# Kernel optimization log

Measured on AMD Instinct MI355X. Metric: run time of the kernel, lower is better.

## Reference

```python
import jax, jax.numpy as jnp
import numpy as np

DIM = 512
HEADS = 16
DIM_HEAD = 64
INNER = HEADS * DIM_HEAD
MAX_T = 32
BASE = 10000.0


def rotate_half(t):
    t1, t2 = jnp.split(t, 2, axis=-1)
    return jnp.concatenate((-t2, t1), axis=-1)


def setup_inputs() -> dict:
    key = jax.random.key(0)
    ks = jax.random.split(key, 12)
    B, T, S = 2, 16, 128
    x = jax.random.normal(ks[0], (B, T, S, DIM), dtype=jnp.float32)
    y = jax.random.normal(ks[1], (B, T, S, DIM), dtype=jnp.float32)
    temporal_mask = jax.random.randint(ks[2], (B, T, T), 0, 2).astype(jnp.int32)
    sc = 1.0 / np.sqrt(DIM)
    Wq = jax.random.normal(ks[3], (DIM, INNER), dtype=jnp.float32) * sc
    Wk = jax.random.normal(ks[4], (DIM, INNER), dtype=jnp.float32) * sc
    Wv = jax.random.normal(ks[5], (DIM, INNER), dtype=jnp.float32) * sc
    Wo = jax.random.normal(ks[6], (INNER, DIM), dtype=jnp.float32) / np.sqrt(INNER)
    bo = jnp.zeros((DIM,), dtype=jnp.float32)
    pos_emb = jax.random.normal(ks[7], (MAX_T, DIM), dtype=jnp.float32)
    gate_w = jax.random.normal(ks[8], (DIM, 1), dtype=jnp.float32) * sc
    gate_b = jnp.zeros((1,), dtype=jnp.float32)
    return {"x": x, "y": y, "temporal_mask": temporal_mask, "Wq": Wq, "Wk": Wk,
            "Wv": Wv, "Wo": Wo, "bo": bo, "pos_emb": pos_emb,
            "gate_w": gate_w, "gate_b": gate_b}


def reference(x, y, temporal_mask, Wq, Wk, Wv, Wo, bo, pos_emb, gate_w, gate_b):
    B, T, S, D = x.shape
    n = T * S
    scale = DIM_HEAD ** (-0.5)
    # temporal positional embedding (T <= MAX_T path)
    tp = pos_emb[:T][None, :, None, :]  # [1,T,1,D]
    x = x + tp
    y = y + tp
    xf = x.reshape(B, n, D)
    yf = y.reshape(B, n, D)
    # NOTE: k is computed from x (as in the source), v from y
    q = (xf @ Wq).reshape(B, n, HEADS, DIM_HEAD).transpose(0, 2, 1, 3)
    k = (xf @ Wk).reshape(B, n, HEADS, DIM_HEAD).transpose(0, 2, 1, 3)
    v = (yf @ Wv).reshape(B, n, HEADS, DIM_HEAD).transpose(0, 2, 1, 3)
    # RoPE over flattened token index
    inv_freq = 1.0 / (BASE ** (jnp.arange(0, DIM_HEAD, 2, dtype=jnp.float32) / DIM_HEAD))
    freqs = jnp.arange(n, dtype=jnp.float32)[:, None] * inv_freq[None, :]  # [n, d/2]
    emb = jnp.concatenate((freqs, freqs), axis=-1)  # [n, d]
    fc = jnp.cos(emb)[None, None, :, :]
    fs = jnp.sin(emb)[None, None, :, :]
    q = q * fc + rotate_half(q) * fs
    k = k * fc + rotate_half(k) * fs
    dots = jnp.einsum('bhid,bhjd->bhij', q, k) * scale  # [B,H,n,n]
    # expand temporal mask [B,T,T] -> [B,1,n,n] block structure
    m = jnp.repeat(jnp.repeat(temporal_mask, S, axis=1), S, axis=2)[:, None, :, :]
    dots = jnp.where(m == 0, -jnp.inf, dots)
    attn = jax.nn.softmax(dots, axis=-1)
    out = jnp.einsum('bhij,bhjd->bhid', attn, v)  # [B,H,n,d]
    out = out.transpose(0, 2, 1, 3).reshape(B, n, INNER)
    out = out @ Wo + bo
    out = out.reshape(B, T, S, D)
    gate = jax.nn.sigmoid(out @ gate_w + gate_b)  # [B,T,S,1]
    return out * gate
```

## Files before the change

### kernel.cpp

```cpp
#include <hip/hip_runtime.h>
#include <hip/hip_bf16.h>

typedef __attribute__((ext_vector_type(4))) short short4v;
typedef __attribute__((ext_vector_type(8))) short short8v;
typedef __attribute__((ext_vector_type(4))) float float4v;
typedef __attribute__((ext_vector_type(2))) unsigned int uint2v;
typedef __attribute__((ext_vector_type(4))) unsigned int uint4v;

#define NTOK 2048
#define MROWS 4096
#define DMODEL 512
#define NINNER 1024
#define DH 64
#define HH 16
#define LOG2E 1.4426950408889634f

__device__ __forceinline__ unsigned short b2s(float f) {
    __hip_bfloat16 h = __float2bfloat16(f);
    return __builtin_bit_cast(unsigned short, h);
}
__device__ __forceinline__ float bf2f(unsigned short h) {
    unsigned int u = ((unsigned int)h) << 16;
    return __builtin_bit_cast(float, u);
}

__device__ __forceinline__ float4v mfma32(short8v a, short8v b, float4v c) {
    return __builtin_amdgcn_mfma_f32_16x16x32_bf16(a, b, c, 0, 0, 0);
}

__device__ __forceinline__ void gld16(const void* g, void* l) {
    __builtin_amdgcn_global_load_lds((const __attribute__((address_space(1))) void*)g,
                                     (__attribute__((address_space(3))) void*)l, 16, 0, 0);
}

__global__ void k_pre(const float* __restrict__ x, const float* __restrict__ y,
                      const float* __restrict__ pe,
                      unsigned short* __restrict__ xpb, unsigned short* __restrict__ ypb,
                      const float* __restrict__ Wq, const float* __restrict__ Wk,
                      const float* __restrict__ Wv, const float* __restrict__ Wo,
                      const float* __restrict__ gwv, const float* __restrict__ gbv,
                      const float* __restrict__ bo,
                      unsigned short* __restrict__ wall, unsigned short* __restrict__ wot,
                      float* __restrict__ ctab, float* __restrict__ stab,
                      unsigned short* __restrict__ gvp, float* __restrict__ bgp) {
    __shared__ float tl[64][65];
    const int blk = blockIdx.x;
    const int tid = threadIdx.x;
    if (blk < 2048) {
        int e0 = (blk * 256 + tid) * 4;
        int row = e0 >> 9, col = e0 & 511;
        int t = (row & (NTOK - 1)) >> 7;
        const float4v xv = *(const float4v*)(x + e0);
        const float4v yv = *(const float4v*)(y + e0);
        const float4v pv = *(const float4v*)(pe + t * DMODEL + col);
        short4v xo, yo;
#pragma unroll
        for (int i = 0; i < 4; ++i) {
            xo[i] = (short)b2s(xv[i] + pv[i]);
            yo[i] = (short)b2s(yv[i] + pv[i]);
        }
        *(short4v*)(xpb + e0) = xo;
        *(short4v*)(ypb + e0) = yo;
    } else if (blk < 2560) {
        int t = blk - 2048;
        const float* W;
        unsigned short* dst;
        int K, N, k0, n0;
        if (t < 384) {
            int which = t / 128, tile = t % 128;
            W = (which == 0) ? Wq : (which == 1) ? Wk : Wv;
            dst = wall + (size_t)which * 1024 * 512;
            K = 512; N = 1024;
            k0 = (tile >> 4) * 64; n0 = (tile & 15) * 64;
        } else {
            int tile = t - 384;
            W = Wo; dst = wot;
            K = 1024; N = 512;
            k0 = (tile >> 3) * 64; n0 = (tile & 7) * 64;
        }
        int tx = tid & 63, ty4 = tid >> 6;
#pragma unroll
        for (int p = 0; p < 16; ++p) {
            int ky = p * 4 + ty4;
            tl[ky][tx] = W[(size_t)(k0 + ky) * N + n0 + tx];
        }
        __syncthreads();
#pragma unroll
        for (int p = 0; p < 16; ++p) {
            int ny = p * 4 + ty4;
            dst[(size_t)(n0 + ny) * K + k0 + tx] = b2s(tl[tx][ny]);
        }
    } else if (blk < 2816) {
        int idx = (blk - 2560) * 256 + tid;
        int p = idx >> 5, j = idx & 31;
        float invf = powf(10000.0f, -(float)(2 * j) * (1.0f / 64.0f));
        float f = (float)p * invf;
        ctab[idx] = cosf(f);
        stab[idx] = sinf(f);
    } else if (blk < 2832) {
        int base = (blk - 2816) * 64;
        int w = tid >> 6, l = tid & 63, l16 = l & 15, g = l >> 4;
        int row = base + w * 16 + l16;
        const float* wr = Wo + (size_t)row * 512 + g * 128;
        const float* gr = gwv + g * 128;
        float s = 0.f;
#pragma unroll
        for (int t = 0; t < 32; ++t) {
            float4v a = *(const float4v*)(wr + t * 4);
            float4v b = *(const float4v*)(gr + t * 4);
            s += a[0] * b[0] + a[1] * b[1] + a[2] * b[2] + a[3] * b[3];
        }
        s += __shfl_xor(s, 16);
        s += __shfl_xor(s, 32);
        if (g == 0) gvp[row] = b2s(s);
    } else {
        if (tid < 64) {
            float s = 0.f;
#pragma unroll
            for (int t = 0; t < 8; ++t) s += bo[tid + t * 64] * gwv[tid + t * 64];
#pragma unroll
            for (int off = 32; off > 0; off >>= 1) s += __shfl_xor(s, off);
            if (tid == 0) bgp[0] = s + gbv[0];
        }
    }
}

__global__ __launch_bounds__(256) void k_qkv(const unsigned short* __restrict__ A,
                                             const unsigned short* __restrict__ A2,
                                             const unsigned short* __restrict__ Bt,
                                             unsigned short* __restrict__ Cq,
                                             unsigned short* __restrict__ Ck,
                                             unsigned short* __restrict__ Cvv,
                                             const float* __restrict__ ctab,
                                             const float* __restrict__ stab,
                                             float scale) {
    __shared__ unsigned short Ab[2][4096];
    __shared__ unsigned short Bb[2][4096];
    const int tid = threadIdx.x;
    const int w = tid >> 6, l = tid & 63, l16 = l & 15, g = l >> 4;
    const int wm = w >> 1, wn = w & 1;
    const int m0 = blockIdx.y * 128, n0 = blockIdx.x * 128;
    const unsigned short* Ap = (n0 >= 2048) ? A2 : A;
    float4v acc[4][4];
#pragma unroll
    for (int i = 0; i < 4; ++i)
#pragma unroll
        for (int j = 0; j < 4; ++j) acc[i][j] = (float4v){0.f, 0.f, 0.f, 0.f};

    auto stage = [&](int t, int buf) {
        int k0 = t * 32;
#pragma unroll
        for (int it = 0; it < 2; ++it) {
            int f = it * 4 + w;
            gld16(Ap + (size_t)(m0 + f * 16 + l16) * 512 + k0 + g * 8, &Ab[buf][f * 512]);
            gld16(Bt + (size_t)(n0 + f * 16 + l16) * 512 + k0 + g * 8, &Bb[buf][f * 512]);
        }
    };

    stage(0, 0);
    __syncthreads();
    for (int t = 0; t < 16; ++t) {
        const int cur = t & 1;
        if (t + 1 < 16) stage(t + 1, cur ^ 1);
        short8v af[4], bf[4];
#pragma unroll
        for (int mi = 0; mi < 4; ++mi)
            af[mi] = *(const short8v*)&Ab[cur][(wm * 4 + mi) * 512 + l * 8];
#pragma unroll
        for (int nj = 0; nj < 4; ++nj)
            bf[nj] = *(const short8v*)&Bb[cur][(wn * 4 + nj) * 512 + l * 8];
        __builtin_amdgcn_s_setprio(1);
#pragma unroll
        for (int mi = 0; mi < 4; ++mi)
#pragma unroll
            for (int nj = 0; nj < 4; ++nj)
                acc[mi][nj] = mfma32(af[mi], bf[nj], acc[mi][nj]);
        __builtin_amdgcn_s_setprio(0);
        __syncthreads();
    }

    const int hh = (n0 + wn * 64) >> 6;
    const int head = hh & 15;
    if (hh < 32) {
        unsigned short* out = (hh < 16) ? Cq : Ck;
        const float sc = (hh < 16) ? scale : 1.0f;
#pragma unroll
        for (int mi = 0; mi < 4; ++mi)
#pragma unroll
            for (int r = 0; r < 4; ++r) {
                int row = m0 + wm * 64 + mi * 16 + g * 4 + r;
                int b = row >> 11, pos = row & (NTOK - 1);
                const float* cr = ctab + pos * 32;
                const float* sr = stab + pos * 32;
                unsigned short* ob = out + (size_t)((b * HH + head) * NTOK + pos) * DH;
#pragma unroll
                for (int nj = 0; nj < 2; ++nj) {
                    int j = nj * 16 + l16;
                    float c = cr[j], s = sr[j];
                    float v1 = acc[mi][nj][r], v2 = acc[mi][nj + 2][r];
                    ob[j] = b2s((v1 * c - v2 * s) * sc);
                    ob[j + 32] = b2s((v2 * c + v1 * s) * sc);
                }
            }
    } else {
#pragma unroll
        for (int mi = 0; mi < 4; ++mi)
#pragma unroll
            for (int nj = 0; nj < 4; ++nj) {
                int d = nj * 16 + l16;
                int row0 = m0 + wm * 64 + mi * 16 + g * 4;
                int b = row0 >> 11, pos0 = row0 & (NTOK - 1);
                short4v o;
#pragma unroll
                for (int r = 0; r < 4; ++r) o[r] = (short)b2s(acc[mi][nj][r]);
                *(short4v*)(Cvv + (size_t)((b * HH + head) * DH + d) * NTOK + pos0) = o;
            }
    }
}

__global__ __launch_bounds__(256) void k_oproj(const unsigned short* __restrict__ A,
                                               const unsigned short* __restrict__ Bt,
                                               const float* __restrict__ bo,
                                               const unsigned short* __restrict__ gv,
                                               const float* __restrict__ bgp,
                                               float* __restrict__ out) {
    __shared__ unsigned short Ab[2][4096];
    __shared__ unsigned short Bb[2][2048];
    __shared__ float glds[128];
    const int tid = threadIdx.x;
    const int w = tid >> 6, l = tid & 63, l16 = l & 15, g = l >> 4;
    const int m0 = blockIdx.y * 128, n0 = blockIdx.x * 64;
    float4v acc[2][4];
#pragma unroll
    for (int i = 0; i < 2; ++i)
#pragma unroll
        for (int j = 0; j < 4; ++j) acc[i][j] = (float4v){0.f, 0.f, 0.f, 0.f};
    float gp0 = 0.f, gp1 = 0.f;

    auto stage = [&](int t, int buf) {
        int k0 = t * 32;
#pragma unroll
        for (int s = 0; s < 2; ++s) {
            int fi = s * 4 + w;
            gld16(A + (size_t)(m0 + fi * 16 + l16) * 1024 + k0 + g * 8, &Ab[buf][fi * 512]);
        }
        gld16(Bt + (size_t)(n0 + w * 16 + l16) * 1024 + k0 + g * 8, &Bb[buf][w * 512]);
    };

    stage(0, 0);
    __syncthreads();
    for (int t = 0; t < 32; ++t) {
        const int cur = t & 1;
        if (t + 1 < 32) stage(t + 1, cur ^ 1);
        short8v af[2], bf[4];
#pragma unroll
        for (int mi = 0; mi < 2; ++mi)
            af[mi] = *(const short8v*)&Ab[cur][(w * 2 + mi) * 512 + l * 8];
#pragma unroll
        for (int nj = 0; nj < 4; ++nj)
            bf[nj] = *(const short8v*)&Bb[cur][nj * 512 + l * 8];
        short8v gvv = *(const short8v*)(gv + t * 32 + g * 8);
        __builtin_amdgcn_s_setprio(1);
#pragma unroll
        for (int mi = 0; mi < 2; ++mi)
#pragma unroll
            for (int nj = 0; nj < 4; ++nj)
                acc[mi][nj] = mfma32(af[mi], bf[nj], acc[mi][nj]);
        __builtin_amdgcn_s_setprio(0);
#pragma unroll
        for (int j = 0; j < 8; ++j) {
            float gf = bf2f((unsigned short)gvv[j]);
            gp0 = fmaf(bf2f((unsigned short)af[0][j]), gf, gp0);
            gp1 = fmaf(bf2f((unsigned short)af[1][j]), gf, gp1);
        }
        __syncthreads();
    }
    gp0 += __shfl_xor(gp0, 16); gp0 += __shfl_xor(gp0, 32);
    gp1 += __shfl_xor(gp1, 16); gp1 += __shfl_xor(gp1, 32);
    const float bg = bgp[0];
    if (g == 0) {
        glds[w * 32 + l16] = 1.0f / (1.0f + __expf(-(gp0 + bg)));
        glds[w * 32 + 16 + l16] = 1.0f / (1.0f + __expf(-(gp1 + bg)));
    }
    __syncthreads();
#pragma unroll
    for (int mi = 0; mi < 2; ++mi)
#pragma unroll
        for (int nj = 0; nj < 4; ++nj) {
            int col = n0 + nj * 16 + l16;
            float bv = bo[col];
#pragma unroll
            for (int r = 0; r < 4; ++r) {
                int row = m0 + w * 32 + mi * 16 + g * 4 + r;
                float gt = glds[w * 32 + mi * 16 + g * 4 + r];
                out[(size_t)row * 512 + col] = (acc[mi][nj][r] + bv) * gt;
            }
        }
}

__global__ __launch_bounds__(512) void k_attn(const unsigned short* __restrict__ qh,
                                              const unsigned short* __restrict__ kh,
                                              const unsigned short* __restrict__ vt,
                                              const int* __restrict__ tmask,
                                              unsigned short* __restrict__ otmp) {
    __shared__ unsigned short Kb[2][8192];
    __shared__ unsigned short Vb[2][8192];
    __shared__ int tlist[17];
    const int blk = blockIdx.x;
    const int u = (blk & 7) * 64 + (blk >> 3);
    const int ti = u & 15, h = (u >> 4) & 15, b = u >> 8;
    const int tid = threadIdx.x, w = tid >> 6, l = tid & 63, l16 = l & 15, g = l >> 4;
    if (tid == 0) {
        int c = 0;
        for (int j = 0; j < 16; ++j)
            if (tmask[(b * 16 + ti) * 16 + j]) tlist[c++] = j;
        tlist[16] = c;
    }
    __syncthreads();
    const int cnt = tlist[16];
    const unsigned short* qb = qh + (size_t)((b * HH + h) * NTOK) * DH;
    const unsigned short* kb = kh + (size_t)((b * HH + h) * NTOK) * DH;
    const unsigned short* vb = vt + (size_t)((b * HH + h) * DH) * NTOK;
    const int q0 = ti * 128 + w * 16;

    short8v qf[2];
#pragma unroll
    for (int c = 0; c < 2; ++c)
        qf[c] = *(const short8v*)(qb + (size_t)(q0 + l16) * DH + c * 32 + g * 8);

    float4v oacc[4];
#pragma unroll
    for (int i = 0; i < 4; ++i) oacc[i] = (float4v){0.f, 0.f, 0.f, 0.f};
    float mx = -1e30f, lrow = 0.f;
    uint4v vrg[2];

    auto stageK = [&](int tj, int buf) {
#pragma unroll
        for (int s = 0; s < 2; ++s) {
            int fi = w * 2 + s;
            const unsigned short* ga =
                kb + (size_t)(tj * 128 + (fi >> 1) * 16 + l16) * DH + (fi & 1) * 32 + g * 8;
            gld16(ga, &Kb[buf][fi * 512]);
        }
    };
    auto loadV = [&](int tj) {
#pragma unroll
        for (int s = 0; s < 2; ++s) {
            int fi = w * 2 + s;
            const unsigned short* ga =
                vb + (size_t)((fi >> 2) * 16 + l16) * NTOK + tj * 128 + (fi & 3) * 32 + g * 4;
            uint2v lo = *(const uint2v*)ga;
            uint2v hi = *(const uint2v*)(ga + 16);
            vrg[s] = (uint4v){lo[0], lo[1], hi[0], hi[1]};
        }
    };
    auto writeV = [&](int buf) {
#pragma unroll
        for (int s = 0; s < 2; ++s)
            *(uint4v*)&Vb[buf][(w * 2 + s) * 512 + l * 8] = vrg[s];
    };

    if (cnt > 0) {
        stageK(tlist[0], 0);
        loadV(tlist[0]);
        writeV(0);
        __syncthreads();
        for (int i = 0; i < cnt; ++i) {
            const int cur = i & 1;
            const bool pre = (i + 1 < cnt);
            if (pre) { stageK(tlist[i + 1], cur ^ 1); loadV(tlist[i + 1]); }
            float4v sacc[8];
#pragma unroll
            for (int jk = 0; jk < 8; ++jk) sacc[jk] = (float4v){0.f, 0.f, 0.f, 0.f};
            __builtin_amdgcn_s_setprio(1);
#pragma unroll
            for (int jk = 0; jk < 8; ++jk) {
                short8v kf0 = *(const short8v*)&Kb[cur][(jk * 2 + 0) * 512 + l * 8];
                short8v kf1 = *(const short8v*)&Kb[cur][(jk * 2 + 1) * 512 + l * 8];
                sacc[jk] = mfma32(kf0, qf[0], sacc[jk]);
                sacc[jk] = mfma32(kf1, qf[1], sacc[jk]);
            }
            __builtin_amdgcn_s_setprio(0);
            float tm = -1e30f;
#pragma unroll
            for (int jk = 0; jk < 8; ++jk) {
                float4v s4 = sacc[jk];
                tm = fmaxf(tm, fmaxf(fmaxf(s4[0], s4[1]), fmaxf(s4[2], s4[3])));
            }
            tm = fmaxf(tm, __shfl_xor(tm, 16));
            tm = fmaxf(tm, __shfl_xor(tm, 32));
            if (!__all(tm <= mx + 8.0f)) {
                float mnew = fmaxf(mx, tm);
                float alpha = exp2f(mx - mnew);
                lrow *= alpha;
#pragma unroll
                for (int md = 0; md < 4; ++md)
#pragma unroll
                    for (int r = 0; r < 4; ++r) oacc[md][r] *= alpha;
                mx = mnew;
            }
            short8v pf[4];
            float4v tsv = {0.f, 0.f, 0.f, 0.f};
#pragma unroll
            for (int cc = 0; cc < 4; ++cc) {
                float p[8];
#pragma unroll
                for (int r = 0; r < 4; ++r) {
                    p[r] = exp2f(sacc[2 * cc][r] - mx);
                    p[r + 4] = exp2f(sacc[2 * cc + 1][r] - mx);
                }
                short8v pv;
#pragma unroll
                for (int r = 0; r < 4; ++r) {
                    tsv[r] += p[r] + p[r + 4];
                    pv[r] = (short)b2s(p[r]);
                    pv[r + 4] = (short)b2s(p[r + 4]);
                }
                pf[cc] = pv;
            }
            float ts = (tsv[0] + tsv[1]) + (tsv[2] + tsv[3]);
            ts += __shfl_xor(ts, 16);
            ts += __shfl_xor(ts, 32);
            lrow += ts;
            if (pre) writeV(cur ^ 1);
            __builtin_amdgcn_s_setprio(1);
#pragma unroll
            for (int md = 0; md < 4; ++md)
#pragma unroll
                for (int cc = 0; cc < 4; ++cc) {
                    short8v vf = *(const short8v*)&Vb[cur][(md * 4 + cc) * 512 + l * 8];
                    oacc[md] = mfma32(vf, pf[cc], oacc[md]);
                }
            __builtin_amdgcn_s_setprio(0);
            __syncthreads();
        }
    }
    float inv = lrow > 0.f ? 1.0f / lrow : 0.f;
    int q = q0 + l16;
#pragma unroll
    for (int md = 0; md < 4; ++md) {
        short4v o;
#pragma unroll
        for (int r = 0; r < 4; ++r) o[r] = (short)b2s(oacc[md][r] * inv);
        *(short4v*)(otmp + (size_t)(b * NTOK + q) * NINNER + h * DH + md * 16 + g * 4) = o;
    }
}

extern "C" void kernel_launch(void* const* d_in, const int* in_sizes, int n_in,
                              void* d_out, int out_size, void* d_ws, size_t ws_size,
                              hipStream_t stream) {
    (void)in_sizes; (void)n_in; (void)out_size; (void)ws_size;
    const float* x = (const float*)d_in[0];
    const float* y = (const float*)d_in[1];
    const int* tmask = (const int*)d_in[2];
    const float* Wq = (const float*)d_in[3];
    const float* Wk = (const float*)d_in[4];
    const float* Wv = (const float*)d_in[5];
    const float* Wo = (const float*)d_in[6];
    const float* bo = (const float*)d_in[7];
    const float* pe = (const float*)d_in[8];
    const float* gw = (const float*)d_in[9];
    const float* gb = (const float*)d_in[10];

    char* ws = (char*)d_ws;
    const size_t MB = 1u << 20;
    unsigned short* xpb  = (unsigned short*)(ws + 0);
    unsigned short* ypb  = (unsigned short*)(ws + 4 * MB);
    unsigned short* wall = (unsigned short*)(ws + 8 * MB);
    unsigned short* wot  = (unsigned short*)(ws + 11 * MB);
    unsigned short* qh   = (unsigned short*)(ws + 12 * MB);
    unsigned short* kh   = (unsigned short*)(ws + 20 * MB);
    unsigned short* vt   = (unsigned short*)(ws + 28 * MB);
    unsigned short* otm  = (unsigned short*)(ws + 36 * MB);
    float* ct = (float*)(ws + 44 * MB);
    float* st = (float*)(ws + 44 * MB + 256 * 1024);
    unsigned short* gv = (unsigned short*)(ws + 45 * MB);
    float* bg = (float*)(ws + 45 * MB + 4096);
    float* outp = (float*)d_out;

    k_pre<<<2833, 256, 0, stream>>>(x, y, pe, xpb, ypb, Wq, Wk, Wv, Wo, gw, gb, bo,
                                    wall, wot, ct, st, gv, bg);
    k_qkv<<<dim3(24, 32), 256, 0, stream>>>(xpb, ypb, wall, qh, kh, vt, ct, st,
                                            0.125f * LOG2E);
    k_attn<<<512, 512, 0, stream>>>(qh, kh, vt, tmask, otm);
    k_oproj<<<dim3(8, 32), 256, 0, stream>>>(otm, wot, bo, gv, bg, outp);
}
```

Baseline: 135.6 us.

## Halve attention KV tile to 64 keys and split gate dot into separate kernel

The attention kernel now streams K/V in 64-key sub-tiles, two per allowed temporal block, instead of 128-key tiles. This halves shared-memory use and per-iteration register pressure, which may allow more resident waves, at the cost of twice as many loop iterations and barriers. The gate logit computation is moved out of the output-projection GEMM loop into a new small kernel that writes per-row sigmoid values. This removes redundant gate FMAs that were repeated across the 8 column blocks, but adds a kernel launch and an extra read of the attention output.

```diff
diff --git a/kernel.cpp b/kernel.cpp
--- a/kernel.cpp
+++ b/kernel.cpp
@@ -218,15 +218,34 @@
     }
 }
 
+__global__ __launch_bounds__(256) void k_gatev(const unsigned short* __restrict__ otm,
+                                               const unsigned short* __restrict__ gv,
+                                               const float* __restrict__ bgp,
+                                               float* __restrict__ glog) {
+    int row = blockIdx.x * 4 + (threadIdx.x >> 6);
+    int l = threadIdx.x & 63;
+    const unsigned short* pr = otm + (size_t)row * NINNER;
+    float acc = 0.f;
+#pragma unroll
+    for (int c = 0; c < 2; ++c) {
+        short8v a = *(const short8v*)(pr + (c * 64 + l) * 8);
+        short8v b = *(const short8v*)(gv + (c * 64 + l) * 8);
+#pragma unroll
+        for (int j = 0; j < 8; ++j)
+            acc = fmaf(bf2f((unsigned short)a[j]), bf2f((unsigned short)b[j]), acc);
+    }
+#pragma unroll
+    for (int off = 32; off > 0; off >>= 1) acc += __shfl_xor(acc, off);
+    if (l == 0) glog[row] = 1.0f / (1.0f + __expf(-(acc + bgp[0])));
+}
+
 __global__ __launch_bounds__(256) void k_oproj(const unsigned short* __restrict__ A,
                                                const unsigned short* __restrict__ Bt,
                                                const float* __restrict__ bo,
-                                               const unsigned short* __restrict__ gv,
-                                               const float* __restrict__ bgp,
+                                               const float* __restrict__ glog,
                                                float* __restrict__ out) {
     __shared__ unsigned short Ab[2][4096];
     __shared__ unsigned short Bb[2][2048];
-    __shared__ float glds[128];
     const int tid = threadIdx.x;
     const int w = tid >> 6, l = tid & 63, l16 = l & 15, g = l >> 4;
     const int m0 = blockIdx.y * 128, n0 = blockIdx.x * 64;
@@ -235,7 +254,6 @@
     for (int i = 0; i < 2; ++i)
 #pragma unroll
         for (int j = 0; j < 4; ++j) acc[i][j] = (float4v){0.f, 0.f, 0.f, 0.f};
-    float gp0 = 0.f, gp1 = 0.f;
 
     auto stage = [&](int t, int buf) {
         int k0 = t * 32;
@@ -259,7 +277,6 @@
 #pragma unroll
         for (int nj = 0; nj < 4; ++nj)
             bf[nj] = *(const short8v*)&Bb[cur][nj * 512 + l * 8];
-        short8v gvv = *(const short8v*)(gv + t * 32 + g * 8);
         __builtin_amdgcn_s_setprio(1);
 #pragma unroll
         for (int mi = 0; mi < 2; ++mi)
@@ -267,24 +284,14 @@
             for (int nj = 0; nj < 4; ++nj)
                 acc[mi][nj] = mfma32(af[mi], bf[nj], acc[mi][nj]);
         __builtin_amdgcn_s_setprio(0);
-#pragma unroll
-        for (int j = 0; j < 8; ++j) {
-            float gf = bf2f((unsigned short)gvv[j]);
-            gp0 = fmaf(bf2f((unsigned short)af[0][j]), gf, gp0);
-            gp1 = fmaf(bf2f((unsigned short)af[1][j]), gf, gp1);
-        }
         __syncthreads();
     }
-    gp0 += __shfl_xor(gp0, 16); gp0 += __shfl_xor(gp0, 32);
-    gp1 += __shfl_xor(gp1, 16); gp1 += __shfl_xor(gp1, 32);
-    const float bg = bgp[0];
-    if (g == 0) {
-        glds[w * 32 + l16] = 1.0f / (1.0f + __expf(-(gp0 + bg)));
-        glds[w * 32 + 16 + l16] = 1.0f / (1.0f + __expf(-(gp1 + bg)));
-    }
-    __syncthreads();
-#pragma unroll
-    for (int mi = 0; mi < 2; ++mi)
+#pragma unroll
+    for (int mi = 0; mi < 2; ++mi) {
+        float gl[4];
+#pragma unroll
+        for (int r = 0; r < 4; ++r)
+            gl[r] = glog[m0 + w * 32 + mi * 16 + g * 4 + r];
 #pragma unroll
         for (int nj = 0; nj < 4; ++nj) {
             int col = n0 + nj * 16 + l16;
@@ -292,10 +299,10 @@
 #pragma unroll
             for (int r = 0; r < 4; ++r) {
                 int row = m0 + w * 32 + mi * 16 + g * 4 + r;
-                float gt = glds[w * 32 + mi * 16 + g * 4 + r];
-                out[(size_t)row * 512 + col] = (acc[mi][nj][r] + bv) * gt;
-            }
-        }
+                out[(size_t)row * 512 + col] = (acc[mi][nj][r] + bv) * gl[r];
+            }
+        }
+    }
 }
 
 __global__ __launch_bounds__(512) void k_attn(const unsigned short* __restrict__ qh,
@@ -303,9 +310,9 @@
                                               const unsigned short* __restrict__ vt,
                                               const int* __restrict__ tmask,
                                               unsigned short* __restrict__ otmp) {
-    __shared__ unsigned short Kb[2][8192];
-    __shared__ unsigned short Vb[2][8192];
-    __shared__ int tlist[17];
+    __shared__ unsigned short Kb[2][4096];
+    __shared__ unsigned short Vb[2][4096];
+    __shared__ int tlist[33];
     const int blk = blockIdx.x;
     const int u = (blk & 7) * 64 + (blk >> 3);
     const int ti = u & 15, h = (u >> 4) & 15, b = u >> 8;
@@ -313,11 +320,11 @@
     if (tid == 0) {
         int c = 0;
         for (int j = 0; j < 16; ++j)
-            if (tmask[(b * 16 + ti) * 16 + j]) tlist[c++] = j;
-        tlist[16] = c;
+            if (tmask[(b * 16 + ti) * 16 + j]) { tlist[c++] = 2 * j; tlist[c++] = 2 * j + 1; }
+        tlist[32] = c;
     }
     __syncthreads();
-    const int cnt = tlist[16];
+    const int cnt = tlist[32];
     const unsigned short* qb = qh + (size_t)((b * HH + h) * NTOK) * DH;
     const unsigned short* kb = kh + (size_t)((b * HH + h) * NTOK) * DH;
     const unsigned short* vb = vt + (size_t)((b * HH + h) * DH) * NTOK;
@@ -332,32 +339,22 @@
 #pragma unroll
     for (int i = 0; i < 4; ++i) oacc[i] = (float4v){0.f, 0.f, 0.f, 0.f};
     float mx = -1e30f, lrow = 0.f;
-    uint4v vrg[2];
-
-    auto stageK = [&](int tj, int buf) {
-#pragma unroll
-        for (int s = 0; s < 2; ++s) {
-            int fi = w * 2 + s;
-            const unsigned short* ga =
-                kb + (size_t)(tj * 128 + (fi >> 1) * 16 + l16) * DH + (fi & 1) * 32 + g * 8;
-            gld16(ga, &Kb[buf][fi * 512]);
-        }
+    uint4v vrg;
+
+    auto stageK = [&](int st, int buf) {
+        const unsigned short* ga =
+            kb + (size_t)(st * 64 + (w >> 1) * 16 + l16) * DH + (w & 1) * 32 + g * 8;
+        gld16(ga, &Kb[buf][w * 512]);
     };
-    auto loadV = [&](int tj) {
-#pragma unroll
-        for (int s = 0; s < 2; ++s) {
-            int fi = w * 2 + s;
-            const unsigned short* ga =
-                vb + (size_t)((fi >> 2) * 16 + l16) * NTOK + tj * 128 + (fi & 3) * 32 + g * 4;
-            uint2v lo = *(const uint2v*)ga;
-            uint2v hi = *(const uint2v*)(ga + 16);
-            vrg[s] = (uint4v){lo[0], lo[1], hi[0], hi[1]};
-        }
+    auto loadV = [&](int st) {
+        const unsigned short* ga =
+            vb + (size_t)((w >> 1) * 16 + l16) * NTOK + st * 64 + (w & 1) * 32 + g * 4;
+        uint2v lo = *(const uint2v*)ga;
+        uint2v hi = *(const uint2v*)(ga + 16);
+        vrg = (uint4v){lo[0], lo[1], hi[0], hi[1]};
     };
     auto writeV = [&](int buf) {
-#pragma unroll
-        for (int s = 0; s < 2; ++s)
-            *(uint4v*)&Vb[buf][(w * 2 + s) * 512 + l * 8] = vrg[s];
+        *(uint4v*)&Vb[buf][w * 512 + l * 8] = vrg;
     };
 
     if (cnt > 0) {
@@ -369,12 +366,12 @@
             const int cur = i & 1;
             const bool pre = (i + 1 < cnt);
             if (pre) { stageK(tlist[i + 1], cur ^ 1); loadV(tlist[i + 1]); }
-            float4v sacc[8];
-#pragma unroll
-            for (int jk = 0; jk < 8; ++jk) sacc[jk] = (float4v){0.f, 0.f, 0.f, 0.f};
+            float4v sacc[4];
+#pragma unroll
+            for (int jk = 0; jk < 4; ++jk) sacc[jk] = (float4v){0.f, 0.f, 0.f, 0.f};
             __builtin_amdgcn_s_setprio(1);
 #pragma unroll
-            for (int jk = 0; jk < 8; ++jk) {
+            for (int jk = 0; jk < 4; ++jk) {
                 short8v kf0 = *(const short8v*)&Kb[cur][(jk * 2 + 0) * 512 + l * 8];
                 short8v kf1 = *(const short8v*)&Kb[cur][(jk * 2 + 1) * 512 + l * 8];
                 sacc[jk] = mfma32(kf0, qf[0], sacc[jk]);
@@ -383,7 +380,7 @@
             __builtin_amdgcn_s_setprio(0);
             float tm = -1e30f;
 #pragma unroll
-            for (int jk = 0; jk < 8; ++jk) {
+            for (int jk = 0; jk < 4; ++jk) {
                 float4v s4 = sacc[jk];
                 tm = fmaxf(tm, fmaxf(fmaxf(s4[0], s4[1]), fmaxf(s4[2], s4[3])));
             }
@@ -399,10 +396,10 @@
                     for (int r = 0; r < 4; ++r) oacc[md][r] *= alpha;
                 mx = mnew;
             }
-            short8v pf[4];
+            short8v pf[2];
             float4v tsv = {0.f, 0.f, 0.f, 0.f};
 #pragma unroll
-            for (int cc = 0; cc < 4; ++cc) {
+            for (int cc = 0; cc < 2; ++cc) {
                 float p[8];
 #pragma unroll
                 for (int r = 0; r < 4; ++r) {
@@ -427,8 +424,8 @@
 #pragma unroll
             for (int md = 0; md < 4; ++md)
 #pragma unroll
-                for (int cc = 0; cc < 4; ++cc) {
-                    short8v vf = *(const short8v*)&Vb[cur][(md * 4 + cc) * 512 + l * 8];
+                for (int cc = 0; cc < 2; ++cc) {
+                    short8v vf = *(const short8v*)&Vb[cur][(md * 2 + cc) * 512 + l * 8];
                     oacc[md] = mfma32(vf, pf[cc], oacc[md]);
                 }
             __builtin_amdgcn_s_setprio(0);
@@ -476,6 +473,7 @@
     float* st = (float*)(ws + 44 * MB + 256 * 1024);
     unsigned short* gv = (unsigned short*)(ws + 45 * MB);
     float* bg = (float*)(ws + 45 * MB + 4096);
+    float* glog = (float*)(ws + 45 * MB + 8192);
     float* outp = (float*)d_out;
 
     k_pre<<<2833, 256, 0, stream>>>(x, y, pe, xpb, ypb, Wq, Wk, Wv, Wo, gw, gb, bo,
@@ -483,5 +481,6 @@
     k_qkv<<<dim3(24, 32), 256, 0, stream>>>(xpb, ypb, wall, qh, kh, vt, ct, st,
                                             0.125f * LOG2E);
     k_attn<<<512, 512, 0, stream>>>(qh, kh, vt, tmask, otm);
-    k_oproj<<<dim3(8, 32), 256, 0, stream>>>(otm, wot, bo, gv, bg, outp);
-}
+    k_gatev<<<1024, 256, 0, stream>>>(otm, gv, bg, glog);
+    k_oproj<<<dim3(8, 32), 256, 0, stream>>>(otm, wot, bo, glog, outp);
+}
```

Measured after the change: 133.0 us. No clear change (-1.9%).
